# Kernel optimization log

Hardware: AMD Instinct MI355X
Metric: run time of the kernel (lower is better)

## Reference

```python
import jax, jax.numpy as jnp
import numpy as np

B, T, D, H, L, FF, SPLIT = 2, 4096, 256, 4 * 0 + 8, 4, 1024, 2048
HD = D // H
EPS = 1e-5


def _layernorm(x, s, b):
    mu = jnp.mean(x, axis=-1, keepdims=True)
    var = jnp.mean(jnp.square(x - mu), axis=-1, keepdims=True)
    return (x - mu) * jax.lax.rsqrt(var + EPS) * s + b


def setup_inputs() -> dict:
    key = jax.random.key(0)
    ks = jax.random.split(key, 10)
    sc = 0.02
    inp = {
        "rows": jax.random.normal(ks[0], (B, T, D), jnp.float32),
        "train_target_embeddings": jax.random.normal(ks[1], (B, SPLIT, D), jnp.float32),
        "Wq": sc * jax.random.normal(ks[2], (L, D, D), jnp.float32),
        "bq": jnp.zeros((L, D), jnp.float32),
        "Wk": sc * jax.random.normal(ks[3], (L, D, D), jnp.float32),
        "bk": jnp.zeros((L, D), jnp.float32),
        "Wv": sc * jax.random.normal(ks[4], (L, D, D), jnp.float32),
        "bv": jnp.zeros((L, D), jnp.float32),
        "Wo": sc * jax.random.normal(ks[5], (L, D, D), jnp.float32),
        "bo": jnp.zeros((L, D), jnp.float32),
        "W1": sc * jax.random.normal(ks[6], (L, D, FF), jnp.float32),
        "b1": jnp.zeros((L, FF), jnp.float32),
        "W2": sc * jax.random.normal(ks[7], (L, FF, D), jnp.float32),
        "b2": jnp.zeros((L, D), jnp.float32),
        "ln1_s": jnp.ones((L, D), jnp.float32),
        "ln1_b": jnp.zeros((L, D), jnp.float32),
        "ln2_s": jnp.ones((L, D), jnp.float32),
        "ln2_b": jnp.zeros((L, D), jnp.float32),
        "split": SPLIT,
    }
    return inp


def reference(rows, train_target_embeddings, Wq, bq, Wk, bk, Wv, bv, Wo, bo,
              W1, b1, W2, b2, ln1_s, ln1_b, ln2_s, ln2_b, split):
    # residual add of train target embeddings onto the train rows
    x = rows.at[:, :split, :].add(train_target_embeddings)
    t = x.shape[1]
    # allowed mask: every query can see all train columns; test queries also see themselves
    key_is_train = jnp.arange(t) < split                      # [T]
    allowed = key_is_train[None, :] | jnp.eye(t, dtype=bool)  # [T,T]
    neg = jnp.asarray(-1e9, x.dtype)
    scale = 1.0 / np.sqrt(HD)
    n_layers = Wq.shape[0]
    for l in range(n_layers):
        # multi-head attention with structured mask
        q = (x @ Wq[l] + bq[l]).reshape(x.shape[0], t, H, HD)
        k = (x @ Wk[l] + bk[l]).reshape(x.shape[0], t, H, HD)
        v = (x @ Wv[l] + bv[l]).reshape(x.shape[0], t, H, HD)
        logits = jnp.einsum('bqhd,bkhd->bhqk', q, k) * scale
        logits = jnp.where(allowed[None, None], logits, neg)
        attn = jax.nn.softmax(logits, axis=-1)
        o = jnp.einsum('bhqk,bkhd->bqhd', attn, v).reshape(x.shape[0], t, D)
        x = _layernorm(x + (o @ Wo[l] + bo[l]), ln1_s[l], ln1_b[l])
        # feed-forward
        h = jax.nn.gelu(x @ W1[l] + b1[l])
        x = _layernorm(x + (h @ W2[l] + b2[l]), ln2_s[l], ln2_b[l])
    return x
```

## Files before the change

kernel.cpp:

```cpp
#include <hip/hip_runtime.h>
#include <cstdint>
#include <cstddef>

#define TSEQ 4096
#define BATCH 2
#define DIM 256
#define NHEAD 8
#define HDIM 32
#define NLAYER 4
#define FFDIM 1024
#define SPLITN 2048
#define MROWS (BATCH * TSEQ)

#define QSCALE 0.2550784545f

typedef __attribute__((ext_vector_type(4))) float f32x4;
typedef __attribute__((ext_vector_type(8))) short bf16x8;

__device__ __forceinline__ short f2bf(float f) {
  union { float f; uint32_t u; } v; v.f = f;
  uint32_t r = v.u + 0x7fffu + ((v.u >> 16) & 1u);
  return (short)(r >> 16);
}

__device__ __forceinline__ float bf2f(short s) {
  union { uint32_t u; float f; } v; v.u = ((uint32_t)(uint16_t)s) << 16;
  return v.f;
}

__device__ __forceinline__ float fast_exp2(float x) {
#if __has_builtin(__builtin_amdgcn_exp2f)
  return __builtin_amdgcn_exp2f(x);
#else
  float r;
  asm volatile("v_exp_f32 %0, %1\n\ts_nop 1" : "=v"(r) : "v"(x));
  return r;
#endif
}

__device__ __forceinline__ uint32_t pack2bf(float a, float b) {
  union { float f; uint32_t u; } ua, ub; ua.f = a; ub.f = b;
  return ((ua.u + 0x8000u) >> 16) | ((ub.u + 0x8000u) & 0xffff0000u);
}

__device__ __forceinline__ bf16x8 mk8(uint32_t a, uint32_t b, uint32_t c, uint32_t d) {
  union { uint32_t u[4]; bf16x8 v; } x; x.u[0] = a; x.u[1] = b; x.u[2] = c; x.u[3] = d;
  return x.v;
}

__device__ __forceinline__ float gelu_f(float x) {
  float u = 0.7978845608f * x * (1.0f + 0.044715f * x * x);
  u = fminf(fmaxf(u, -20.f), 20.f);
  float e = fast_exp2(2.885390082f * u);
  float t = (e - 1.0f) / (e + 1.0f);
  return 0.5f * x * (1.0f + t);
}

#define AS1 __attribute__((address_space(1)))
#define AS3 __attribute__((address_space(3)))
__device__ __forceinline__ void gload16(const void* g, void* l) {
  __builtin_amdgcn_global_load_lds((AS1 void*)g, (AS3 void*)l, 16, 0, 0);
}

__global__ __launch_bounds__(256) void prep_w(
    const float* __restrict__ Wq, const float* __restrict__ Wk,
    const float* __restrict__ Wv, const float* __restrict__ Wo,
    const float* __restrict__ W1, const float* __restrict__ W2,
    short* __restrict__ qkvT, short* __restrict__ woT,
    short* __restrict__ w1T, short* __restrict__ w2T)
{
  const int NQKV = NLAYER * 768 * DIM;
  const int NO   = NLAYER * DIM * DIM;
  const int NF   = NLAYER * FFDIM * DIM;
  const int total = NQKV + NO + 2 * NF;
  for (int idx = blockIdx.x * 256 + threadIdx.x; idx < total; idx += gridDim.x * 256) {
    if (idx < NQKV) {
      const int l = idx / (768 * DIM);
      const int rem = idx - l * 768 * DIM;
      const int n = rem >> 8, k = rem & 255;
      const float* src = (n < 256) ? Wq : ((n < 512) ? Wk : Wv);
      qkvT[idx] = f2bf(src[((size_t)l * DIM + k) * DIM + (n & 255)]);
    } else if (idx < NQKV + NO) {
      const int j = idx - NQKV;
      const int l = j >> 16;
      const int rem = j & 65535;
      const int n = rem >> 8, k = rem & 255;
      woT[j] = f2bf(Wo[((size_t)l * DIM + k) * DIM + n]);
    } else if (idx < NQKV + NO + NF) {
      const int j = idx - NQKV - NO;
      const int l = j >> 18;
      const int rem = j & 262143;
      const int n = rem >> 8, k = rem & 255;
      w1T[j] = f2bf(W1[((size_t)l * DIM + k) * FFDIM + n]);
    } else {
      const int j = idx - NQKV - NO - NF;
      const int l = j >> 18;
      const int rem = j & 262143;
      const int n = rem >> 10, k = rem & 1023;
      w2T[j] = f2bf(W2[((size_t)l * FFDIM + k) * DIM + n]);
    }
  }
}

__global__ __launch_bounds__(256) void prep_x(
    const float* __restrict__ rows, const float* __restrict__ tte,
    float* __restrict__ xf, short* __restrict__ xb)
{
  const size_t idx = (size_t)blockIdx.x * 256 + threadIdx.x;
  float4 v = ((const float4*)rows)[idx];
  const size_t e = idx * 4;
  const int m = (int)(e >> 8);
  const int d = (int)(e & 255);
  const int t = m & (TSEQ - 1);
  const int bb = m >> 12;
  if (t < SPLITN) {
    const float4 a = ((const float4*)tte)[((size_t)bb * SPLITN + t) * (DIM / 4) + (d >> 2)];
    v.x += a.x; v.y += a.y; v.z += a.z; v.w += a.w;
  }
  ((float4*)xf)[idx] = v;
  short4 pk; pk.x = f2bf(v.x); pk.y = f2bf(v.y); pk.z = f2bf(v.z); pk.w = f2bf(v.w);
  ((short4*)xb)[idx] = pk;
}

#define GBM 128
#define GBN 64
#define GBK 64

template<int EPI>
__global__ __launch_bounds__(256, 4) void gemm_bt(
    const short* __restrict__ A, const short* __restrict__ BT,
    const float* __restrict__ bias0, const float* __restrict__ bias1,
    const float* __restrict__ bias2, void* __restrict__ Cout,
    int M, int N, int K)
{
  __shared__ short As[GBM * GBK];
  __shared__ short Bs[GBN * GBK];
  const int tid = threadIdx.x;
  const int lane = tid & 63;
  const int wave = tid >> 6;
  const int wm = wave & 1, wn = wave >> 1;
  const int col = lane & 15, quad = lane >> 4;

  const short* Ab = A + (size_t)blockIdx.x * GBM * K;
  const short* Bb = BT + (size_t)blockIdx.y * GBN * K;

  const f32x4 fz = {0.f, 0.f, 0.f, 0.f};
  f32x4 acc[4][2];
#pragma unroll
  for (int i = 0; i < 4; ++i)
#pragma unroll
    for (int j = 0; j < 2; ++j) acc[i][j] = fz;

  for (int k0 = 0; k0 < K; k0 += GBK) {
#pragma unroll
    for (int p = 0; p < 4; ++p) {
      const int i = p * 256 + tid;
      const int r = i >> 3, g = i & 7;
      gload16(Ab + (size_t)r * K + k0 + ((g ^ (r & 7)) * 8), &As[i * 8]);
    }
#pragma unroll
    for (int p = 0; p < 2; ++p) {
      const int i = p * 256 + tid;
      const int r = i >> 3, g = i & 7;
      gload16(Bb + (size_t)r * K + k0 + ((g ^ (r & 7)) * 8), &Bs[i * 8]);
    }
    __syncthreads();
#pragma unroll
    for (int ks = 0; ks < GBK; ks += 32) {
      bf16x8 af[4], bfr[2];
      const int gq = (ks >> 3) + quad;
#pragma unroll
      for (int tm = 0; tm < 4; ++tm) {
        const int row = wm * 64 + tm * 16 + col;
        af[tm] = *(const bf16x8*)&As[row * GBK + ((gq ^ (row & 7)) * 8)];
      }
#pragma unroll
      for (int tn = 0; tn < 2; ++tn) {
        const int row = wn * 32 + tn * 16 + col;
        bfr[tn] = *(const bf16x8*)&Bs[row * GBK + ((gq ^ (row & 7)) * 8)];
      }
#pragma unroll
      for (int tm = 0; tm < 4; ++tm)
#pragma unroll
        for (int tn = 0; tn < 2; ++tn)
          acc[tm][tn] = __builtin_amdgcn_mfma_f32_16x16x32_bf16(af[tm], bfr[tn], acc[tm][tn], 0, 0, 0);
    }
    __syncthreads();
  }

#pragma unroll
  for (int tm = 0; tm < 4; ++tm) {
    const int mbase = blockIdx.x * GBM + wm * 64 + tm * 16 + quad * 4;
#pragma unroll
    for (int tn = 0; tn < 2; ++tn) {
      const int n = blockIdx.y * GBN + wn * 32 + tn * 16 + col;
      float bv;
      if (EPI == 1) bv = (n < 256) ? bias0[n] : ((n < 512) ? bias1[n - 256] : bias2[n - 512]);
      else          bv = bias0[n];
#pragma unroll
      for (int r = 0; r < 4; ++r) {
        float v = acc[tm][tn][r] + bv;
        size_t off = (size_t)(mbase + r) * N + n;
        if (EPI == 1) {
          if (n < 256) v *= QSCALE;
          ((short*)Cout)[off] = f2bf(v);
        } else {
          ((short*)Cout)[off] = f2bf(gelu_f(v));
        }
      }
    }
  }
}

__global__ __launch_bounds__(256, 2) void gemm_ln(
    const short* __restrict__ A,
    const short* __restrict__ BT, const float* __restrict__ bias,
    const float* __restrict__ xres,
    const float* __restrict__ gs, const float* __restrict__ gb,
    float* __restrict__ xoutf, short* __restrict__ xoutb, int K)
{
  __shared__ short As[2][32 * 64];
  __shared__ short Bs[2][256 * 64];
  __shared__ float ssum[4][32], ssq[4][32];
  const int tid = threadIdx.x;
  const int lane = tid & 63;
  const int wave = tid >> 6;
  const int col = lane & 15, quad = lane >> 4;
  const int m0 = blockIdx.x * 32;

  const f32x4 fz = {0.f, 0.f, 0.f, 0.f};
  f32x4 acc[2][4];
#pragma unroll
  for (int i = 0; i < 2; ++i)
#pragma unroll
    for (int j = 0; j < 4; ++j) acc[i][j] = fz;

  const int arow = tid >> 3;
  const int agr  = tid & 7;
  const int grow = m0 + arow;
  const int asw  = (agr ^ (arow & 7)) * 8;

#define STAGE_B(k0_, buf_) do {                                              \
    _Pragma("unroll")                                                        \
    for (int p_ = 0; p_ < 8; ++p_) {                                         \
      const int i_ = p_ * 256 + tid;                                         \
      const int r_ = i_ >> 3, g_ = i_ & 7;                                   \
      gload16(BT + (size_t)r_ * K + (k0_) + ((g_ ^ (r_ & 7)) * 8),           \
              &Bs[buf_][i_ * 8]);                                            \
    } } while (0)

#define STAGE_A(k0_, buf_)                                                   \
    gload16(A + (size_t)grow * K + (k0_) + asw, &As[buf_][tid * 8])

  const int NT = K / 64;
  STAGE_B(0, 0);
  STAGE_A(0, 0);
  __syncthreads();

  int cur = 0;
  for (int t = 0; t < NT; ++t) {
    if (t + 1 < NT) {
      STAGE_B((t + 1) * 64, cur ^ 1);
      STAGE_A((t + 1) * 64, cur ^ 1);
    }
#pragma unroll
    for (int ks = 0; ks < 64; ks += 32) {
      bf16x8 af[2], bfr[4];
      const int gq = (ks >> 3) + quad;
#pragma unroll
      for (int tm = 0; tm < 2; ++tm) {
        const int row = tm * 16 + col;
        af[tm] = *(const bf16x8*)&As[cur][row * 64 + ((gq ^ (row & 7)) * 8)];
      }
#pragma unroll
      for (int tn = 0; tn < 4; ++tn) {
        const int row = wave * 64 + tn * 16 + col;
        bfr[tn] = *(const bf16x8*)&Bs[cur][row * 64 + ((gq ^ (row & 7)) * 8)];
      }
#pragma unroll
      for (int tm = 0; tm < 2; ++tm)
#pragma unroll
        for (int tn = 0; tn < 4; ++tn)
          acc[tm][tn] = __builtin_amdgcn_mfma_f32_16x16x32_bf16(af[tm], bfr[tn], acc[tm][tn], 0, 0, 0);
    }
    __syncthreads();
    cur ^= 1;
  }
#undef STAGE_B
#undef STAGE_A

  const float* resb = xres + (size_t)m0 * DIM;
#pragma unroll
  for (int tn = 0; tn < 4; ++tn) {
    const int n = wave * 64 + tn * 16 + col;
    const float bv = bias[n];
#pragma unroll
    for (int tm = 0; tm < 2; ++tm)
#pragma unroll
      for (int r = 0; r < 4; ++r) {
        const int row = tm * 16 + quad * 4 + r;
        acc[tm][tn][r] += bv + resb[(size_t)row * DIM + n];
      }
  }

#pragma unroll
  for (int tm = 0; tm < 2; ++tm)
#pragma unroll
    for (int r = 0; r < 4; ++r) {
      float s = 0.f, q = 0.f;
#pragma unroll
      for (int tn = 0; tn < 4; ++tn) { const float v = acc[tm][tn][r]; s += v; q += v * v; }
      s += __shfl_xor(s, 1); q += __shfl_xor(q, 1);
      s += __shfl_xor(s, 2); q += __shfl_xor(q, 2);
      s += __shfl_xor(s, 4); q += __shfl_xor(q, 4);
      s += __shfl_xor(s, 8); q += __shfl_xor(q, 8);
      if (col == 0) { const int row = tm * 16 + quad * 4 + r; ssum[wave][row] = s; ssq[wave][row] = q; }
    }
  __syncthreads();
  if (tid < 32) {
    const float S = ssum[0][tid] + ssum[1][tid] + ssum[2][tid] + ssum[3][tid];
    const float Q = ssq[0][tid] + ssq[1][tid] + ssq[2][tid] + ssq[3][tid];
    const float mu = S * (1.0f / DIM);
    const float var = Q * (1.0f / DIM) - mu * mu;
    ssum[0][tid] = mu;
    ssq[0][tid] = rsqrtf(var + 1e-5f);
  }
  __syncthreads();

#pragma unroll
  for (int tm = 0; tm < 2; ++tm)
#pragma unroll
    for (int tn = 0; tn < 4; ++tn) {
      const int n = wave * 64 + tn * 16 + col;
      const float g = gs[n], bb = gb[n];
#pragma unroll
      for (int r = 0; r < 4; ++r) {
        const int row = tm * 16 + quad * 4 + r;
        const float out = (acc[tm][tn][r] - ssum[0][row]) * ssq[0][row] * g + bb;
        xoutf[(size_t)(m0 + row) * DIM + n] = out;
        xoutb[(size_t)(m0 + row) * DIM + n] = f2bf(out);
      }
    }
}

#define AKT 64
#define NKT (SPLITN / AKT)

__global__ __launch_bounds__(256, 4) void attn_kernel(
    const short* __restrict__ qkv, short* __restrict__ ob)
{
  __shared__ short Kbuf[2][AKT * HDIM];
  __shared__ short Vbuf[2][HDIM * AKT];
  __shared__ float Pdiag[4][16];

  const int tid = threadIdx.x;
  const int lane = tid & 63;
  const int wave = tid >> 6;
  const int col = lane & 15, quad = lane >> 4;
  const int bh = blockIdx.y;
  const int b = bh >> 3, h = bh & 7;
  const int q0 = blockIdx.x * 128 + wave * 32;

  const short* qbase = qkv + (size_t)b * TSEQ * 768 + h * HDIM;
  const short* kbase = qbase + 256;
  const short* vcol  = qbase + 512;

  const short* ksrc = kbase + (size_t)(tid & 63) * 768 + (tid >> 6) * 8;
  const int vkey = tid & 63, vhg = tid >> 6;
  const int vs = vkey >> 4, vqd = (vkey >> 2) & 3, vrr = vkey & 3;
  const int vpos = (vs >> 1) * 32 + vqd * 8 + (vs & 1) * 4 + vrr;
  const int vgs = vpos >> 3, vo8 = vpos & 7;
  const short* vsrc = vcol + (size_t)vkey * 768 + vhg * 8;

  const bf16x8 qf0 = *(const bf16x8*)(qbase + (size_t)(q0 + col) * 768 + quad * 8);
  const bf16x8 qf1 = *(const bf16x8*)(qbase + (size_t)(q0 + 16 + col) * 768 + quad * 8);

  bf16x8 ones;
#pragma unroll
  for (int i = 0; i < 8; ++i) ones[i] = (short)0x3F80;

  const f32x4 fz = {0.f, 0.f, 0.f, 0.f};
  f32x4 o[2][2] = {{fz, fz}, {fz, fz}};
  f32x4 lacc[2] = {fz, fz};

  gload16(ksrc, &Kbuf[0][tid * 8]);
  {
    const bf16x8 v0 = *(const bf16x8*)vsrc;
#pragma unroll
    for (int j = 0; j < 8; ++j)
      Vbuf[0][(vhg * 8 + j) * 64 + ((vgs ^ j) * 8) + vo8] = v0[j];
  }
  bf16x8 vnext = *(const bf16x8*)(vsrc + (size_t)AKT * 768);

  int cur = 0;
  for (int t = 0; t < NKT; ++t) {
    __syncthreads();
    if (t + 1 < NKT) {
      gload16(ksrc + (size_t)(t + 1) * AKT * 768, &Kbuf[1 - cur][tid * 8]);
#pragma unroll
      for (int j = 0; j < 8; ++j)
        Vbuf[1 - cur][(vhg * 8 + j) * 64 + ((vgs ^ j) * 8) + vo8] = vnext[j];
      if (t + 2 < NKT) vnext = *(const bf16x8*)(vsrc + (size_t)(t + 2) * AKT * 768);
    }
    const short* kb = Kbuf[cur];
    const short* vb = Vbuf[cur];

    uint32_t pw0[8], pw1[8];
#pragma unroll
    for (int st = 0; st < 4; ++st) {
      const bf16x8 kf = *(const bf16x8*)&kb[(quad * 64 + st * 16 + col) * 8];
      const f32x4 s0 = __builtin_amdgcn_mfma_f32_16x16x32_bf16(kf, qf0, fz, 0, 0, 0);
      const f32x4 s1 = __builtin_amdgcn_mfma_f32_16x16x32_bf16(kf, qf1, fz, 0, 0, 0);
      pw0[st * 2]     = pack2bf(fast_exp2(s0[0]), fast_exp2(s0[1]));
      pw0[st * 2 + 1] = pack2bf(fast_exp2(s0[2]), fast_exp2(s0[3]));
      pw1[st * 2]     = pack2bf(fast_exp2(s1[0]), fast_exp2(s1[1]));
      pw1[st * 2 + 1] = pack2bf(fast_exp2(s1[2]), fast_exp2(s1[3]));
    }

#pragma unroll
    for (int kh = 0; kh < 2; ++kh) {
      const bf16x8 pf0 = mk8(pw0[kh * 4], pw0[kh * 4 + 1], pw0[kh * 4 + 2], pw0[kh * 4 + 3]);
      const bf16x8 pf1 = mk8(pw1[kh * 4], pw1[kh * 4 + 1], pw1[kh * 4 + 2], pw1[kh * 4 + 3]);
#pragma unroll
      for (int hh = 0; hh < 2; ++hh) {
        const int hd = hh * 16 + col;
        const bf16x8 vf = *(const bf16x8*)&vb[hd * AKT + (((kh * 4 + quad) ^ (hd & 7)) * 8)];
        o[0][hh] = __builtin_amdgcn_mfma_f32_16x16x32_bf16(pf0, vf, o[0][hh], 0, 0, 0);
        o[1][hh] = __builtin_amdgcn_mfma_f32_16x16x32_bf16(pf1, vf, o[1][hh], 0, 0, 0);
      }
      lacc[0] = __builtin_amdgcn_mfma_f32_16x16x32_bf16(pf0, ones, lacc[0], 0, 0, 0);
      lacc[1] = __builtin_amdgcn_mfma_f32_16x16x32_bf16(pf1, ones, lacc[1], 0, 0, 0);
    }
    cur ^= 1;
  }

  if (blockIdx.x >= SPLITN / 128) {
#pragma unroll
    for (int qsub = 0; qsub < 2; ++qsub) {
      const int qd = q0 + qsub * 16;
      const bf16x8 qf = qsub ? qf1 : qf0;
      const bf16x8 kf = *(const bf16x8*)(kbase + (size_t)(qd + col) * 768 + quad * 8);
      const f32x4 sd = __builtin_amdgcn_mfma_f32_16x16x32_bf16(kf, qf, fz, 0, 0, 0);
      float ps = 0.f;
#pragma unroll
      for (int r = 0; r < 4; ++r)
        if (quad * 4 + r == col) ps = fast_exp2(sd[r]);
      if (quad == (col >> 2)) Pdiag[wave][col] = ps;
      asm volatile("s_waitcnt lgkmcnt(0)" ::: "memory");
      const f32x4 pv = *(const f32x4*)&Pdiag[wave][quad * 4];
#pragma unroll
      for (int r = 0; r < 4; ++r) {
        lacc[qsub][r] += pv[r];
        const size_t vrow = (size_t)(qd + quad * 4 + r) * 768;
#pragma unroll
        for (int hh = 0; hh < 2; ++hh)
          o[qsub][hh][r] += pv[r] * bf2f(vcol[vrow + hh * 16 + col]);
      }
      asm volatile("s_waitcnt lgkmcnt(0)" ::: "memory");
    }
  }

#pragma unroll
  for (int qsub = 0; qsub < 2; ++qsub) {
#pragma unroll
    for (int r = 0; r < 4; ++r) {
      const float inv = 1.0f / lacc[qsub][r];
      const size_t row = (size_t)b * TSEQ + q0 + qsub * 16 + quad * 4 + r;
#pragma unroll
      for (int hh = 0; hh < 2; ++hh)
        ob[row * DIM + h * HDIM + hh * 16 + col] = f2bf(o[qsub][hh][r] * inv);
    }
  }
}

extern "C" void kernel_launch(void* const* d_in, const int* in_sizes, int n_in,
                              void* d_out, int out_size, void* d_ws, size_t ws_size,
                              hipStream_t stream)
{
  const float* rows = (const float*)d_in[0];
  const float* tte  = (const float*)d_in[1];
  const float* Wq = (const float*)d_in[2];  const float* bq = (const float*)d_in[3];
  const float* Wk = (const float*)d_in[4];  const float* bk = (const float*)d_in[5];
  const float* Wv = (const float*)d_in[6];  const float* bv = (const float*)d_in[7];
  const float* Wo = (const float*)d_in[8];  const float* bo = (const float*)d_in[9];
  const float* W1 = (const float*)d_in[10]; const float* b1 = (const float*)d_in[11];
  const float* W2 = (const float*)d_in[12]; const float* b2 = (const float*)d_in[13];
  const float* ln1s = (const float*)d_in[14]; const float* ln1b = (const float*)d_in[15];
  const float* ln2s = (const float*)d_in[16]; const float* ln2b = (const float*)d_in[17];

  char* p = (char*)d_ws;
  float* xf   = (float*)p;  p += (size_t)MROWS * DIM * 4;
  short* xb   = (short*)p;  p += (size_t)MROWS * DIM * 2;
  short* qkv  = (short*)p;  p += (size_t)MROWS * 768 * 2;
  short* hb   = (short*)p;  p += (size_t)MROWS * FFDIM * 2;
  short* ob   = (short*)p;  p += (size_t)MROWS * DIM * 2;
  short* qkvT = (short*)p;  p += (size_t)NLAYER * 768 * DIM * 2;
  short* woT  = (short*)p;  p += (size_t)NLAYER * DIM * DIM * 2;
  short* w1T  = (short*)p;  p += (size_t)NLAYER * FFDIM * DIM * 2;
  short* w2T  = (short*)p;  p += (size_t)NLAYER * DIM * FFDIM * 2;

  prep_w<<<2048, 256, 0, stream>>>(Wq, Wk, Wv, Wo, W1, W2, qkvT, woT, w1T, w2T);
  prep_x<<<MROWS * DIM / 4 / 256, 256, 0, stream>>>(rows, tte, xf, xb);

  for (int l = 0; l < NLAYER; ++l) {
    gemm_bt<1><<<dim3(MROWS / GBM, 768 / GBN), 256, 0, stream>>>(
        xb, qkvT + (size_t)l * 768 * DIM, bq + l * DIM, bk + l * DIM, bv + l * DIM,
        qkv, MROWS, 768, DIM);
    attn_kernel<<<dim3(TSEQ / 128, BATCH * NHEAD), 256, 0, stream>>>(qkv, ob);
    gemm_ln<<<MROWS / 32, 256, 0, stream>>>(
        ob, woT + (size_t)l * DIM * DIM, bo + l * DIM, xf,
        ln1s + l * DIM, ln1b + l * DIM, xf, xb, DIM);
    gemm_bt<3><<<dim3(MROWS / GBM, FFDIM / GBN), 256, 0, stream>>>(
        xb, w1T + (size_t)l * FFDIM * DIM, b1 + l * FFDIM, nullptr, nullptr,
        hb, MROWS, FFDIM, DIM);
    float* xo = (l == NLAYER - 1) ? (float*)d_out : xf;
    gemm_ln<<<MROWS / 32, 256, 0, stream>>>(
        hb, w2T + (size_t)l * DIM * FFDIM,
        b2 + l * DIM, xf, ln2s + l * DIM, ln2b + l * DIM, xo, xb, FFDIM);
  }
}
```

Before: 479.6 us.

## Load full K=256 panels into LDS once and shrink GEMM tile to 64x64

The bias GEMM for QKV and FF1 now stages the whole K=256 depth of the A and B tiles into shared memory in a single pass, so the K loop with a sync per step is gone. The output tile drops from 128x64 to 64x64, which doubles the grid, and launch bounds move from 4 to 2 blocks per CU. The aim is fewer barriers and more blocks in flight. In exchange each block uses 64 KB of LDS, which limits occupancy, and global loads no longer overlap with MFMA work inside a block.

```diff
diff --git a/kernel.cpp b/kernel.cpp
--- a/kernel.cpp
+++ b/kernel.cpp
@@ -122,78 +122,76 @@
   ((short4*)xb)[idx] = pk;
 }
 
-#define GBM 128
-#define GBN 64
-#define GBK 64
+#define GKM 64
+#define GKN 64
+#define KFULL 256
 
 template<int EPI>
-__global__ __launch_bounds__(256, 4) void gemm_bt(
+__global__ __launch_bounds__(256, 2) void gemm_bt(
     const short* __restrict__ A, const short* __restrict__ BT,
     const float* __restrict__ bias0, const float* __restrict__ bias1,
     const float* __restrict__ bias2, void* __restrict__ Cout,
     int M, int N, int K)
 {
-  __shared__ short As[GBM * GBK];
-  __shared__ short Bs[GBN * GBK];
+  __shared__ short As[GKM * KFULL];
+  __shared__ short Bs[GKN * KFULL];
   const int tid = threadIdx.x;
   const int lane = tid & 63;
   const int wave = tid >> 6;
   const int wm = wave & 1, wn = wave >> 1;
   const int col = lane & 15, quad = lane >> 4;
 
-  const short* Ab = A + (size_t)blockIdx.x * GBM * K;
-  const short* Bb = BT + (size_t)blockIdx.y * GBN * K;
+  const short* Ab = A + (size_t)blockIdx.x * GKM * KFULL;
+  const short* Bb = BT + (size_t)blockIdx.y * GKN * KFULL;
+
+#pragma unroll
+  for (int p = 0; p < 8; ++p) {
+    const int i = p * 256 + tid;
+    const int r = i >> 5, g = i & 31;
+    gload16(Ab + (size_t)r * KFULL + ((g ^ (r & 7)) * 8), &As[i * 8]);
+  }
+#pragma unroll
+  for (int p = 0; p < 8; ++p) {
+    const int i = p * 256 + tid;
+    const int r = i >> 5, g = i & 31;
+    gload16(Bb + (size_t)r * KFULL + ((g ^ (r & 7)) * 8), &Bs[i * 8]);
+  }
+  __syncthreads();
 
   const f32x4 fz = {0.f, 0.f, 0.f, 0.f};
-  f32x4 acc[4][2];
-#pragma unroll
-  for (int i = 0; i < 4; ++i)
+  f32x4 acc[2][2];
+#pragma unroll
+  for (int i = 0; i < 2; ++i)
 #pragma unroll
     for (int j = 0; j < 2; ++j) acc[i][j] = fz;
 
-  for (int k0 = 0; k0 < K; k0 += GBK) {
-#pragma unroll
-    for (int p = 0; p < 4; ++p) {
-      const int i = p * 256 + tid;
-      const int r = i >> 3, g = i & 7;
-      gload16(Ab + (size_t)r * K + k0 + ((g ^ (r & 7)) * 8), &As[i * 8]);
-    }
-#pragma unroll
-    for (int p = 0; p < 2; ++p) {
-      const int i = p * 256 + tid;
-      const int r = i >> 3, g = i & 7;
-      gload16(Bb + (size_t)r * K + k0 + ((g ^ (r & 7)) * 8), &Bs[i * 8]);
-    }
-    __syncthreads();
-#pragma unroll
-    for (int ks = 0; ks < GBK; ks += 32) {
-      bf16x8 af[4], bfr[2];
-      const int gq = (ks >> 3) + quad;
-#pragma unroll
-      for (int tm = 0; tm < 4; ++tm) {
-        const int row = wm * 64 + tm * 16 + col;
-        af[tm] = *(const bf16x8*)&As[row * GBK + ((gq ^ (row & 7)) * 8)];
-      }
-#pragma unroll
-      for (int tn = 0; tn < 2; ++tn) {
-        const int row = wn * 32 + tn * 16 + col;
-        bfr[tn] = *(const bf16x8*)&Bs[row * GBK + ((gq ^ (row & 7)) * 8)];
-      }
-#pragma unroll
-      for (int tm = 0; tm < 4; ++tm)
-#pragma unroll
-        for (int tn = 0; tn < 2; ++tn)
-          acc[tm][tn] = __builtin_amdgcn_mfma_f32_16x16x32_bf16(af[tm], bfr[tn], acc[tm][tn], 0, 0, 0);
-    }
-    __syncthreads();
-  }
-
-#pragma unroll
-  for (int tm = 0; tm < 4; ++tm) {
-    const int mbase = blockIdx.x * GBM + wm * 64 + tm * 16 + quad * 4;
+#pragma unroll
+  for (int ks = 0; ks < KFULL; ks += 32) {
+    const int gq = (ks >> 3) + quad;
+    bf16x8 af[2], bfr[2];
+#pragma unroll
+    for (int tm = 0; tm < 2; ++tm) {
+      const int row = wm * 32 + tm * 16 + col;
+      af[tm] = *(const bf16x8*)&As[row * KFULL + ((gq ^ (row & 7)) * 8)];
+    }
 #pragma unroll
     for (int tn = 0; tn < 2; ++tn) {
-      const int n = blockIdx.y * GBN + wn * 32 + tn * 16 + col;
+      const int row = wn * 32 + tn * 16 + col;
+      bfr[tn] = *(const bf16x8*)&Bs[row * KFULL + ((gq ^ (row & 7)) * 8)];
+    }
+#pragma unroll
+    for (int tm = 0; tm < 2; ++tm)
+#pragma unroll
+      for (int tn = 0; tn < 2; ++tn)
+        acc[tm][tn] = __builtin_amdgcn_mfma_f32_16x16x32_bf16(af[tm], bfr[tn], acc[tm][tn], 0, 0, 0);
+  }
+
+#pragma unroll
+  for (int tm = 0; tm < 2; ++tm) {
+    const int mbase = blockIdx.x * GKM + wm * 32 + tm * 16 + quad * 4;
+#pragma unroll
+    for (int tn = 0; tn < 2; ++tn) {
+      const int n = blockIdx.y * GKN + wn * 32 + tn * 16 + col;
       float bv;
       if (EPI == 1) bv = (n < 256) ? bias0[n] : ((n < 512) ? bias1[n - 256] : bias2[n - 512]);
       else          bv = bias0[n];
@@ -503,14 +501,14 @@
   prep_x<<<MROWS * DIM / 4 / 256, 256, 0, stream>>>(rows, tte, xf, xb);
 
   for (int l = 0; l < NLAYER; ++l) {
-    gemm_bt<1><<<dim3(MROWS / GBM, 768 / GBN), 256, 0, stream>>>(
+    gemm_bt<1><<<dim3(MROWS / GKM, 768 / GKN), 256, 0, stream>>>(
         xb, qkvT + (size_t)l * 768 * DIM, bq + l * DIM, bk + l * DIM, bv + l * DIM,
         qkv, MROWS, 768, DIM);
     attn_kernel<<<dim3(TSEQ / 128, BATCH * NHEAD), 256, 0, stream>>>(qkv, ob);
     gemm_ln<<<MROWS / 32, 256, 0, stream>>>(
         ob, woT + (size_t)l * DIM * DIM, bo + l * DIM, xf,
         ln1s + l * DIM, ln1b + l * DIM, xf, xb, DIM);
-    gemm_bt<3><<<dim3(MROWS / GBM, FFDIM / GBN), 256, 0, stream>>>(
+    gemm_bt<3><<<dim3(MROWS / GKM, FFDIM / GKN), 256, 0, stream>>>(
         xb, w1T + (size_t)l * FFDIM * DIM, b1 + l * FFDIM, nullptr, nullptr,
         hb, MROWS, FFDIM, DIM);
     float* xo = (l == NLAYER - 1) ? (float*)d_out : xf;
```

Result: slower. 492.9 us (+2.8%).
